# Kernel tuning notes

Measured on AMD Instinct MI355X. Metric: run time of the kernel, lower is better.

The kernel has to match this reference:

```python
import jax, jax.numpy as jnp
import numpy as np
from jax import lax

THR = 1.0            # spike_threshold
GRAD_WIDTH = 0.5     # sinabs SingleExponential grad_width
GRAD_SCALE = 1.0     # sinabs SingleExponential grad_scale
ABS_WIDTH = THR * GRAD_WIDTH

# SingleSpike with SingleExponential surrogate gradient (Shrestha & Orchard 2018)
@jax.custom_vjp
def spike(v):
    return (v >= THR).astype(v.dtype)

def _spike_fwd(v):
    return (v >= THR).astype(v.dtype), v

def _spike_bwd(v, g):
    sg = (GRAD_SCALE / ABS_WIDTH) * jnp.exp(-jnp.abs(v - THR) / ABS_WIDTH)
    return (g * sg,)

spike.defvjp(_spike_fwd, _spike_bwd)

def avgpool4(x):  # AvgPool2d(4) on NCHW
    n, c, h, w = x.shape
    return x.reshape(n, c, h // 4, 4, w // 4, 4).mean(axis=(3, 5))

def conv7(x, w):  # Conv2d k=7 pad=3 no bias, NCHW/OIHW
    return lax.conv_general_dilated(x, w, (1, 1), [(3, 3), (3, 3)],
                                    dimension_numbers=('NCHW', 'OIHW', 'NCHW'))

def iaf(x):
    """IAF with MembraneSubtract reset. x: (n, t, c, h, w) -> spikes, same shape."""
    xt = jnp.moveaxis(x, 1, 0)  # (t, n, c, h, w)
    def step(v, xin):
        v = v + xin
        s = spike(v)
        return v - s * THR, s
    _, s = lax.scan(step, jnp.zeros_like(xt[0]), xt)
    return jnp.moveaxis(s, 0, 1)

def setup_inputs() -> dict:
    key = jax.random.key(0)
    k0, k1, k2, k3 = jax.random.split(key, 4)
    inp = jax.random.uniform(k0, (8, 2, 256, 256, 64), dtype=jnp.float32)
    w0 = jax.random.normal(k1, (4, 2, 7, 7), jnp.float32) / np.float32(np.sqrt(2 * 49))
    w1 = jax.random.normal(k2, (8, 4, 7, 7), jnp.float32) / np.float32(np.sqrt(4 * 49))
    wl = jax.random.normal(k3, (2, 128), jnp.float32) / np.float32(np.sqrt(128))
    return {"inp": inp, "w0": w0, "w1": w1, "wl": wl}

def reference(inp, w0, w1, wl):
    n, c, y, x, t = inp.shape
    # movedim(-1, 1) then flatten(0, 1): (n, t, c, y, x) -> (n*t, c, y, x)
    data = jnp.moveaxis(inp, -1, 1).reshape(n * t, c, y, x)
    h0 = conv7(avgpool4(data), w0)                          # (n*t, 4, 64, 64)
    s0 = iaf(h0.reshape(n, t, 4, 64, 64)).reshape(n * t, 4, 64, 64)
    h1 = conv7(avgpool4(s0), w1)                            # (n*t, 8, 16, 16)
    s1 = iaf(h1.reshape(n, t, 8, 16, 16)).reshape(n * t, 8, 16, 16)
    feat = avgpool4(s1).reshape(n * t, -1)                  # (n*t, 128)
    out = feat @ wl.T                                       # (n*t, 2)
    return jnp.moveaxis(out.reshape(n, t, 2), 1, -1)        # (n, 2, t)
```

## Files before the change

kernel.cpp:

```cpp
#include <hip/hip_runtime.h>


#define OFF_P0   0
#define OFF_H0   4194304
#define OFF_P1   12582912
#define OFF_H1   13107200
#define OFF_FT   14155776

__global__ void pool0_kernel(const float* __restrict__ inp,
                             float* __restrict__ out) {
    int tid = blockIdx.x * blockDim.x + threadIdx.x;
    int t4 = tid & 15;
    int px = (tid >> 4) & 63;
    int py = (tid >> 10) & 63;
    int nc = tid >> 16;
    const float* base = inp + (size_t)nc * 4194304 + (size_t)t4 * 4;
    int y0 = py * 4, x0 = px * 4;
    double a0 = 0, a1 = 0, a2 = 0, a3 = 0;
    #pragma unroll
    for (int dy = 0; dy < 4; ++dy) {
        const float* row = base + ((size_t)(y0 + dy) * 256 + x0) * 64;
        #pragma unroll
        for (int dx = 0; dx < 4; ++dx) {
            const float4 v = *(const float4*)(row + dx * 64);
            a0 += (double)v.x; a1 += (double)v.y;
            a2 += (double)v.z; a3 += (double)v.w;
        }
    }
    float4 o = make_float4((float)(a0 * 0.0625), (float)(a1 * 0.0625),
                           (float)(a2 * 0.0625), (float)(a3 * 0.0625));
    ((float4*)out)[tid] = o;
}

__global__ void conv0_kernel(const float* __restrict__ pooled0,
                             const float* __restrict__ w0,
                             float* __restrict__ h0) {
    __shared__ double w[392];
    for (int i = threadIdx.x; i < 392; i += blockDim.x) w[i] = (double)w0[i];
    __syncthreads();

    int tid = blockIdx.x * blockDim.x + threadIdx.x;
    int t4  = tid & 15;
    int px  = (tid >> 4) & 63;
    int pyp = (tid >> 10) & 31;
    int n   = tid >> 15;
    int py0 = pyp * 2;

    double acc[4][2][4] = {};
    for (int ic = 0; ic < 2; ++ic) {
        const float* in_c = pooled0 + (size_t)(n * 2 + ic) * 262144 + t4 * 4;
        const double* wic = w + ic * 49;
        #pragma unroll
        for (int r = 0; r < 8; ++r) {
            int iy = py0 - 3 + r;
            if (iy < 0 || iy >= 64) continue;
            const float* in_row = in_c + (size_t)iy * 4096;
            #pragma unroll
            for (int kx = 0; kx < 7; ++kx) {
                int ix = px + kx - 3;
                if (ix < 0 || ix >= 64) continue;
                float4 v = *(const float4*)(in_row + ix * 64);
                if (r <= 6) {
                    #pragma unroll
                    for (int oc = 0; oc < 4; ++oc) {
                        double wd = wic[oc * 98 + r * 7 + kx];
                        acc[oc][0][0] += (double)v.x * wd;
                        acc[oc][0][1] += (double)v.y * wd;
                        acc[oc][0][2] += (double)v.z * wd;
                        acc[oc][0][3] += (double)v.w * wd;
                    }
                }
                if (r >= 1) {
                    #pragma unroll
                    for (int oc = 0; oc < 4; ++oc) {
                        double wd = wic[oc * 98 + (r - 1) * 7 + kx];
                        acc[oc][1][0] += (double)v.x * wd;
                        acc[oc][1][1] += (double)v.y * wd;
                        acc[oc][1][2] += (double)v.z * wd;
                        acc[oc][1][3] += (double)v.w * wd;
                    }
                }
            }
        }
    }
    #pragma unroll
    for (int p = 0; p < 2; ++p) {
        size_t ob = (size_t)n * 1048576 + (size_t)(py0 + p) * 4096
                  + (size_t)px * 64 + t4 * 4;
        #pragma unroll
        for (int oc = 0; oc < 4; ++oc) {
            float4 o = make_float4((float)acc[oc][p][0], (float)acc[oc][p][1],
                                   (float)acc[oc][p][2], (float)acc[oc][p][3]);
            *(float4*)(h0 + ob + (size_t)oc * 262144) = o;
        }
    }
}

__global__ __launch_bounds__(256) void iaf0_pool1_kernel(
        const float* __restrict__ h0, float* __restrict__ pooled1) {
    int b   = blockIdx.x;
    int c   = b & 3;
    int pyo = (b >> 2) & 15;
    int n   = b >> 6;
    int tid = threadIdx.x;
    int dx  = tid & 3;
    int dy  = (tid >> 2) & 3;
    int pxo = tid >> 4;
    int py  = pyo * 4 + dy;
    int px  = pxo * 4 + dx;

    const float4* p = (const float4*)(h0 +
        (((size_t)(n * 4 + c) * 64 + py) * 64 + px) * 64);

    float v = 0.f;
    unsigned int sp[16];
    #pragma unroll
    for (int i = 0; i < 16; ++i) {
        float4 x = p[i];
        unsigned int w = 0;
        #define STEP(j, e)                                                    \
        {   v += x.e;                                                         \
            unsigned int s_ = (v >= 1.f) ? 1u : 0u;                           \
            v -= (float)s_;                                                   \
            w += s_ << (8 * j); }
        STEP(0, x) STEP(1, y) STEP(2, z) STEP(3, w)
        #undef STEP
        sp[i] = w;
    }
    #pragma unroll
    for (int i = 0; i < 16; ++i) {
        sp[i] += __shfl_xor(sp[i], 1);
        sp[i] += __shfl_xor(sp[i], 2);
        sp[i] += __shfl_xor(sp[i], 4);
        sp[i] += __shfl_xor(sp[i], 8);
    }
    int i = tid & 15;
    unsigned int s = sp[i];
    float4 o = make_float4((float)(s & 255u)         * 0.0625f,
                           (float)((s >> 8)  & 255u) * 0.0625f,
                           (float)((s >> 16) & 255u) * 0.0625f,
                           (float)((s >> 24) & 255u) * 0.0625f);
    float* outp = pooled1 + (((size_t)(n * 4 + c) * 16 + pyo) * 16 + pxo) * 64 + i * 4;
    *(float4*)outp = o;
}

__global__ void conv1_kernel(const float* __restrict__ pooled1,
                             const float* __restrict__ w1,
                             float* __restrict__ h1) {
    __shared__ double w[1568];
    for (int i = threadIdx.x; i < 1568; i += blockDim.x) w[i] = (double)w1[i];
    __syncthreads();

    int tid = blockIdx.x * blockDim.x + threadIdx.x;
    int t  = tid & 63;
    int px = (tid >> 6) & 15;
    int py = (tid >> 10) & 15;
    int n  = tid >> 14;
    double acc[8];
    #pragma unroll
    for (int oc = 0; oc < 8; ++oc) acc[oc] = 0.0;

    for (int ic = 0; ic < 4; ++ic) {
        const float* in_c = pooled1 + (size_t)(n * 4 + ic) * 16384;
        const double* wic = w + ic * 49;
        #pragma unroll
        for (int ky = 0; ky < 7; ++ky) {
            int iy = py + ky - 3;
            if (iy < 0 || iy >= 16) continue;
            const float* in_row = in_c + (size_t)iy * 1024 + t;
            const double* wrow = wic + ky * 7;
            #pragma unroll
            for (int kx = 0; kx < 7; ++kx) {
                int ix = px + kx - 3;
                if (ix < 0 || ix >= 16) continue;
                double v = (double)in_row[ix * 64];
                #pragma unroll
                for (int oc = 0; oc < 8; ++oc)
                    acc[oc] += v * wrow[kx + oc * 196];
            }
        }
    }
    size_t ob = (size_t)n * 131072 + (size_t)py * 1024 + px * 64 + t;
    #pragma unroll
    for (int oc = 0; oc < 8; ++oc)
        h1[ob + (size_t)oc * 16384] = (float)acc[oc];
}

__global__ __launch_bounds__(256) void iaf1_pool2_kernel(
        const float* __restrict__ h1, float* __restrict__ feat) {
    int b = blockIdx.x;
    int c = b & 7;
    int n = b >> 3;
    int tid = threadIdx.x;
    int dx  = tid & 3;
    int dy  = (tid >> 2) & 3;
    int q   = tid >> 4;
    int pyo = q >> 2;
    int pxo = q & 3;
    int py  = pyo * 4 + dy;
    int px  = pxo * 4 + dx;

    const float4* p = (const float4*)(h1 +
        (((size_t)(n * 8 + c) * 16 + py) * 16 + px) * 64);

    float v = 0.f;
    unsigned int sp[16];
    #pragma unroll
    for (int i = 0; i < 16; ++i) {
        float4 x = p[i];
        unsigned int w = 0;
        #define STEP(j, e)                                                    \
        {   v += x.e;                                                         \
            unsigned int s_ = (v >= 1.f) ? 1u : 0u;                           \
            v -= (float)s_;                                                   \
            w += s_ << (8 * j); }
        STEP(0, x) STEP(1, y) STEP(2, z) STEP(3, w)
        #undef STEP
        sp[i] = w;
    }
    #pragma unroll
    for (int i = 0; i < 16; ++i) {
        sp[i] += __shfl_xor(sp[i], 1);
        sp[i] += __shfl_xor(sp[i], 2);
        sp[i] += __shfl_xor(sp[i], 4);
        sp[i] += __shfl_xor(sp[i], 8);
    }
    int i = tid & 15;
    unsigned int s = sp[i];
    float4 o = make_float4((float)(s & 255u)         * 0.0625f,
                           (float)((s >> 8)  & 255u) * 0.0625f,
                           (float)((s >> 16) & 255u) * 0.0625f,
                           (float)((s >> 24) & 255u) * 0.0625f);
    int f = c * 16 + q;
    *(float4*)(feat + ((size_t)n * 128 + f) * 64 + i * 4) = o;
}

__global__ __launch_bounds__(64) void linear_kernel(
        const float* __restrict__ feat, const float* __restrict__ wl,
        float* __restrict__ out) {
    int tid = blockIdx.x * 64 + threadIdx.x;
    int t = tid & 63;
    int j = (tid >> 6) & 1;
    int n = tid >> 7;
    const float* fp = feat + (size_t)n * 128 * 64 + t;
    const float* wp = wl + j * 128;
    double acc = 0.0;
    for (int f = 0; f < 128; ++f)
        acc += (double)wp[f] * (double)fp[(size_t)f * 64];
    out[(size_t)(n * 2 + j) * 64 + t] = (float)acc;
}

extern "C" void kernel_launch(void* const* d_in, const int* in_sizes, int n_in,
                              void* d_out, int out_size, void* d_ws, size_t ws_size,
                              hipStream_t stream) {
    const float* inp = (const float*)d_in[0];
    const float* w0  = (const float*)d_in[1];
    const float* w1  = (const float*)d_in[2];
    const float* wl  = (const float*)d_in[3];
    float* out = (float*)d_out;
    float* ws  = (float*)d_ws;

    float* pooled0 = ws + OFF_P0;
    float* h0      = ws + OFF_H0;
    float* pooled1 = ws + OFF_P1;
    float* h1      = ws + OFF_H1;
    float* feat    = ws + OFF_FT;

    pool0_kernel<<<4096, 256, 0, stream>>>(inp, pooled0);
    conv0_kernel<<<1024, 256, 0, stream>>>(pooled0, w0, h0);
    iaf0_pool1_kernel<<<512, 256, 0, stream>>>(h0, pooled1);
    conv1_kernel<<<512, 256, 0, stream>>>(pooled1, w1, h1);
    iaf1_pool2_kernel<<<64, 256, 0, stream>>>(h1, feat);
    linear_kernel<<<16, 64, 0, stream>>>(feat, wl, out);
}
```

Measured before the change: 477.3 us.

## Fuse conv0 with IAF0 and pool1 via shared-memory tile

Merges the first convolution, the first IAF scan and the second average pool into one kernel. Conv outputs are staged in a rotated LDS tile, and half the threads then run the temporal scan and pooling shuffles. This removes writing and rereading the large h0 intermediate in global memory and one kernel launch. In exchange it uses more LDS per block and leaves half the threads idle during the serial scan.

```diff
diff --git a/kernel.cpp b/kernel.cpp
--- a/kernel.cpp
+++ b/kernel.cpp
@@ -2,7 +2,6 @@
 
 
 #define OFF_P0   0
-#define OFF_H0   4194304
 #define OFF_P1   12582912
 #define OFF_H1   13107200
 #define OFF_FT   14155776
@@ -32,19 +31,27 @@
     ((float4*)out)[tid] = o;
 }
 
-__global__ void conv0_kernel(const float* __restrict__ pooled0,
-                             const float* __restrict__ w0,
-                             float* __restrict__ h0) {
+__global__ __launch_bounds__(256) void conv0_iaf0_pool1_kernel(
+        const float* __restrict__ pooled0, const float* __restrict__ w0,
+        float* __restrict__ pooled1) {
     __shared__ double w[392];
+    __shared__ float tile[8192];
+
     for (int i = threadIdx.x; i < 392; i += blockDim.x) w[i] = (double)w0[i];
+
+    int b   = blockIdx.x;
+    int pxb = b & 7;
+    int pyo = (b >> 3) & 15;
+    int n   = b >> 7;
+
+    int tid = threadIdx.x;
+    int t4  = tid & 15;
+    int pxl = (tid >> 4) & 7;
+    int pp  = tid >> 7;
+    int px  = pxb * 8 + pxl;
+    int py0 = pyo * 4 + pp * 2;
+
     __syncthreads();
-
-    int tid = blockIdx.x * blockDim.x + threadIdx.x;
-    int t4  = tid & 15;
-    int px  = (tid >> 4) & 63;
-    int pyp = (tid >> 10) & 31;
-    int n   = tid >> 15;
-    int py0 = pyp * 2;
 
     double acc[4][2][4] = {};
     for (int ic = 0; ic < 2; ++ic) {
@@ -84,64 +91,57 @@
         }
     }
     #pragma unroll
-    for (int p = 0; p < 2; ++p) {
-        size_t ob = (size_t)n * 1048576 + (size_t)(py0 + p) * 4096
-                  + (size_t)px * 64 + t4 * 4;
-        #pragma unroll
-        for (int oc = 0; oc < 4; ++oc) {
-            float4 o = make_float4((float)acc[oc][p][0], (float)acc[oc][p][1],
-                                   (float)acc[oc][p][2], (float)acc[oc][p][3]);
-            *(float4*)(h0 + ob + (size_t)oc * 262144) = o;
-        }
-    }
-}
-
-__global__ __launch_bounds__(256) void iaf0_pool1_kernel(
-        const float* __restrict__ h0, float* __restrict__ pooled1) {
-    int b   = blockIdx.x;
-    int c   = b & 3;
-    int pyo = (b >> 2) & 15;
-    int n   = b >> 6;
-    int tid = threadIdx.x;
-    int dx  = tid & 3;
-    int dy  = (tid >> 2) & 3;
-    int pxo = tid >> 4;
-    int py  = pyo * 4 + dy;
-    int px  = pxo * 4 + dx;
-
-    const float4* p = (const float4*)(h0 +
-        (((size_t)(n * 4 + c) * 64 + py) * 64 + px) * 64);
-
-    float v = 0.f;
-    unsigned int sp[16];
-    #pragma unroll
-    for (int i = 0; i < 16; ++i) {
-        float4 x = p[i];
-        unsigned int w = 0;
-        #define STEP(j, e)                                                    \
-        {   v += x.e;                                                         \
-            unsigned int s_ = (v >= 1.f) ? 1u : 0u;                           \
-            v -= (float)s_;                                                   \
-            w += s_ << (8 * j); }
-        STEP(0, x) STEP(1, y) STEP(2, z) STEP(3, w)
-        #undef STEP
-        sp[i] = w;
-    }
-    #pragma unroll
-    for (int i = 0; i < 16; ++i) {
-        sp[i] += __shfl_xor(sp[i], 1);
-        sp[i] += __shfl_xor(sp[i], 2);
-        sp[i] += __shfl_xor(sp[i], 4);
-        sp[i] += __shfl_xor(sp[i], 8);
-    }
-    int i = tid & 15;
-    unsigned int s = sp[i];
-    float4 o = make_float4((float)(s & 255u)         * 0.0625f,
-                           (float)((s >> 8)  & 255u) * 0.0625f,
-                           (float)((s >> 16) & 255u) * 0.0625f,
-                           (float)((s >> 24) & 255u) * 0.0625f);
-    float* outp = pooled1 + (((size_t)(n * 4 + c) * 16 + pyo) * 16 + pxo) * 64 + i * 4;
-    *(float4*)outp = o;
+    for (int oc = 0; oc < 4; ++oc) {
+        #pragma unroll
+        for (int row = 0; row < 2; ++row) {
+            int p = oc * 32 + (pp * 2 + row) * 8 + pxl;
+            #pragma unroll
+            for (int j = 0; j < 4; ++j) {
+                int tt = t4 * 4 + j;
+                tile[p * 64 + ((tt + p) & 63)] = (float)acc[oc][row][j];
+            }
+        }
+    }
+    __syncthreads();
+
+    if (tid < 128) {
+        int p   = tid;
+        int oc  = p >> 5;
+        int pxo = (p >> 2) & 1;
+        float v = 0.f;
+        unsigned int sp[16];
+        const float* tp = tile + p * 64;
+        #pragma unroll
+        for (int i = 0; i < 16; ++i) {
+            unsigned int wd = 0;
+            #pragma unroll
+            for (int j = 0; j < 4; ++j) {
+                int t = i * 4 + j;
+                float x = tp[(t + p) & 63];
+                v += x;
+                unsigned int s_ = (v >= 1.f) ? 1u : 0u;
+                v -= (float)s_;
+                wd += s_ << (8 * j);
+            }
+            sp[i] = wd;
+        }
+        #pragma unroll
+        for (int i = 0; i < 16; ++i) {
+            sp[i] += __shfl_xor(sp[i], 1);
+            sp[i] += __shfl_xor(sp[i], 2);
+            sp[i] += __shfl_xor(sp[i], 8);
+            sp[i] += __shfl_xor(sp[i], 16);
+        }
+        int i = (p & 3) | (((p >> 3) & 3) << 2);
+        unsigned int s = sp[i];
+        float4 o = make_float4((float)(s & 255u)         * 0.0625f,
+                               (float)((s >> 8)  & 255u) * 0.0625f,
+                               (float)((s >> 16) & 255u) * 0.0625f,
+                               (float)((s >> 24) & 255u) * 0.0625f);
+        float* outp = pooled1 +
+            (((size_t)(n * 4 + oc) * 16 + pyo) * 16 + (pxb * 2 + pxo)) * 64 + i * 4;
+        *(float4*)outp = o;
+    }
 }
 
 __global__ void conv1_kernel(const float* __restrict__ pooled1,
@@ -261,14 +261,12 @@
     float* ws  = (float*)d_ws;
 
     float* pooled0 = ws + OFF_P0;
-    float* h0      = ws + OFF_H0;
     float* pooled1 = ws + OFF_P1;
     float* h1      = ws + OFF_H1;
     float* feat    = ws + OFF_FT;
 
     pool0_kernel<<<4096, 256, 0, stream>>>(inp, pooled0);
-    conv0_kernel<<<1024, 256, 0, stream>>>(pooled0, w0, h0);
-    iaf0_pool1_kernel<<<512, 256, 0, stream>>>(h0, pooled1);
+    conv0_iaf0_pool1_kernel<<<1024, 256, 0, stream>>>(pooled0, w0, pooled1);
     conv1_kernel<<<512, 256, 0, stream>>>(pooled1, w1, h1);
     iaf1_pool2_kernel<<<64, 256, 0, stream>>>(h1, feat);
     linear_kernel<<<16, 64, 0, stream>>>(feat, wl, out);
```

Measured after the change: 466.5 us. -2.3%, faster.
